# Optimization experiments

Hardware: AMD Instinct MI355X
Metric: run time of the kernel (lower is better)

Reference implementation:

```python
import jax, jax.numpy as jnp
import numpy as np

N = 50000          # nodes
E = 800000         # edges (before self-loops)
IN_CH = 16
HID = 32
HEADS = 4
NEG_SLOPE = 0.2    # PyG GATConv default leaky_relu slope


def add_self_loops(edge_index, n):
    loops = jnp.arange(n, dtype=edge_index.dtype)
    return jnp.concatenate([edge_index, jnp.stack([loops, loops])], axis=1)


def gat_layer(x, edge_index, W, a_src, a_dst, bias, heads, out_ch, concat):
    """PyG-style GATConv: gather -> attention logits -> segment softmax over dst -> scatter."""
    n = x.shape[0]
    h = (x @ W).reshape(n, heads, out_ch)            # [N, H, C]
    src, dst = edge_index[0], edge_index[1]          # messages flow src -> dst
    alpha_src = (h * a_src).sum(-1)                  # [N, H]
    alpha_dst = (h * a_dst).sum(-1)                  # [N, H]
    e = jax.nn.leaky_relu(alpha_src[src] + alpha_dst[dst], NEG_SLOPE)  # [Etot, H]
    # numerically stable segment softmax over incoming edges of each dst node
    e_max = jax.ops.segment_max(e, dst, num_segments=n)
    e_exp = jnp.exp(e - e_max[dst])
    denom = jax.ops.segment_sum(e_exp, dst, num_segments=n)
    alpha = e_exp / (denom[dst] + 1e-16)             # [Etot, H]
    out = jax.ops.segment_sum(h[src] * alpha[..., None], dst, num_segments=n)  # [N, H, C]
    out = out.reshape(n, heads * out_ch) if concat else out.mean(axis=1)
    return out + bias


def setup_inputs() -> dict:
    key = jax.random.key(0)
    ks = jax.random.split(key, 10)
    x = jax.random.normal(ks[0], (N, IN_CH), dtype=jnp.float32)
    edge_index = jax.random.randint(ks[1], (2, E), 0, N, dtype=jnp.int64)
    s = 0.1
    W1 = jax.random.normal(ks[2], (IN_CH, HEADS * HID), dtype=jnp.float32) * s
    a_src1 = jax.random.normal(ks[3], (1, HEADS, HID), dtype=jnp.float32) * s
    a_dst1 = jax.random.normal(ks[4], (1, HEADS, HID), dtype=jnp.float32) * s
    b1 = jnp.zeros((HEADS * HID,), dtype=jnp.float32)
    W2 = jax.random.normal(ks[5], (HEADS * HID, 2), dtype=jnp.float32) * s
    a_src2 = jax.random.normal(ks[6], (1, 1, 2), dtype=jnp.float32) * s
    a_dst2 = jax.random.normal(ks[7], (1, 1, 2), dtype=jnp.float32) * s
    b2 = jnp.zeros((2,), dtype=jnp.float32)
    return {"x": x, "edge_index": edge_index,
            "W1": W1, "a_src1": a_src1, "a_dst1": a_dst1, "b1": b1,
            "W2": W2, "a_src2": a_src2, "a_dst2": a_dst2, "b2": b2}


def reference(x, edge_index, W1, a_src1, a_dst1, b1, W2, a_src2, a_dst2, b2):
    ei = add_self_loops(edge_index, x.shape[0])
    h = gat_layer(x, ei, W1, a_src1, a_dst1, b1, HEADS, HID, concat=True)
    h = jax.nn.relu(h)
    out = gat_layer(h, ei, W2, a_src2, a_dst2, b2, 1, 2, concat=False)
    return out
```

## Files before the change

kernel.cpp:

```cpp
#include <hip/hip_runtime.h>
#include <hip/hip_bf16.h>

#define N_NODES 50000
#define N_EDGES 800000
#define ETOT    (N_EDGES + N_NODES)
#define STRIDE  64
#define IN_CH   16
#define HID     32
#define HEADS   4
#define C1      (HEADS * HID)
#define NEG     0.2f
#define NSLICE  8
#define SLICE_N (N_NODES / NSLICE)
#define CAPB    112640

#define DEG_BLOCKS  ((ETOT / 4 + 255) / 256)
#define FILL2_PARTS 110
#define FILL2_BLOCKS (NSLICE * FILL2_PARTS)
#define FILLL_BLOCKS (NSLICE * DEG_BLOCKS)
#define NGROUPS     (N_NODES / 4)
#define H1_BLOCKS   2048

typedef unsigned short u16;
typedef unsigned int   u32;

__device__ __forceinline__ float bf2f(u16 b) {
    return __uint_as_float(((u32)b) << 16);
}

__device__ __forceinline__ u16 f2bf(float f) {
    __hip_bfloat16 hb = __float2bfloat16(f);
    return *(u16*)&hb;
}

__device__ __forceinline__ int clampn(int v) {
    return v < 0 ? 0 : (v >= N_NODES ? N_NODES - 1 : v);
}

__device__ __forceinline__ int eidx(const int* ei, int e, int i64, int which) {
    int v = i64 ? ei[2 * (which * N_EDGES + e)] : ei[which * N_EDGES + e];
    return clampn(v);
}

__device__ __forceinline__ float cvt(const void* src, int i, int bf) {
    return bf ? bf2f(((const u16*)src)[i]) : ((const float*)src)[i];
}

__device__ __forceinline__ int probe_bf_wave(const u16* xb) {
    int l = threadIdx.x & 63;
    int my = 0;
#pragma unroll
    for (int k = 0; k < 4; k++) {
        float f = bf2f(xb[l * 4 + k]);
        float a = fabsf(f);
        if (f == 0.0f || (a > 9.5e-7f && a < 1.05e6f)) my++;
    }
#pragma unroll
    for (int m = 32; m; m >>= 1) my += __shfl_xor(my, m);
    return my >= 224;
}

__device__ __forceinline__ int probe_i64_wave(const int* ei32) {
    int l = threadIdx.x & 63;
    int nz = (l < 32 && ei32[2 * l + 1] != 0) ? 1 : 0;
#pragma unroll
    for (int m = 32; m; m >>= 1) nz += __shfl_xor(nz, m);
    return nz == 0;
}

__device__ __forceinline__ void dev_bucket(const int* __restrict__ ei,
                                           u32* __restrict__ gcnt,
                                           u32* __restrict__ gbuf,
                                           u32* sbuf, u32* scnt, u32* sseg,
                                           u32* sbase, int blk) {
    int i64 = probe_i64_wave(ei);
    if (threadIdx.x < NSLICE) scnt[threadIdx.x] = 0;
    __syncthreads();
    int e0 = (blk * 256 + (int)threadIdx.x) * 4;
    int valid = (e0 < ETOT);
    int bkt[4], pos[4]; u32 pk[4];
    if (valid) {
#pragma unroll
        for (int j = 0; j < 4; j++) {
            int e = e0 + j, s, d;
            if (e < N_EDGES) { s = eidx(ei, e, i64, 0); d = eidx(ei, e, i64, 1); }
            else             { s = d = e - N_EDGES; }
            int b = d / SLICE_N;
            bkt[j] = b;
            pk[j]  = ((u32)s << 16) | (u32)(d - b * SLICE_N);
            pos[j] = (int)atomicAdd(&scnt[b], 1u);
        }
    }
    __syncthreads();
    if (threadIdx.x == 0) {
        u32 run = 0;
        for (int b = 0; b < NSLICE; b++) { sseg[b] = run; run += scnt[b]; }
    }
    __syncthreads();
    if (threadIdx.x < NSLICE)
        sbase[threadIdx.x] = atomicAdd(&gcnt[threadIdx.x * 16], scnt[threadIdx.x]);
    if (valid) {
#pragma unroll
        for (int j = 0; j < 4; j++) sbuf[sseg[bkt[j]] + pos[j]] = pk[j];
    }
    __syncthreads();
#pragma unroll
    for (int b = 0; b < NSLICE; b++) {
        u32 cb = scnt[b], sb = sseg[b], gb = sbase[b];
        for (u32 i = threadIdx.x; i < cb; i += 256) {
            u32 o = gb + i;
            if (o < CAPB) gbuf[(size_t)b * CAPB + o] = sbuf[sb + i];
        }
    }
}

__device__ __forceinline__ void dev_fill2(const u32* __restrict__ gcnt,
                                          const u32* __restrict__ gbuf,
                                          int* __restrict__ degs,
                                          u16* __restrict__ csr, int blk) {
    int s = blk & (NSLICE - 1);
    int part = blk >> 3;
    u32 cnt = gcnt[s * 16]; if (cnt > CAPB) cnt = CAPB;
    u32 i0 = ((u32)part * 256 + (u32)threadIdx.x) * 4;
    if (i0 >= cnt) return;
    const u32* buf = gbuf + (size_t)s * CAPB;
    u32 pk[4]; int nv;
    if (i0 + 4 <= cnt) {
        uint4 q = *(const uint4*)(buf + i0);
        pk[0] = q.x; pk[1] = q.y; pk[2] = q.z; pk[3] = q.w; nv = 4;
    } else {
        nv = (int)(cnt - i0);
#pragma unroll
        for (int j = 0; j < 4; j++) if (j < nv) pk[j] = buf[i0 + j];
    }
    int base = s * SLICE_N;
#pragma unroll
    for (int j = 0; j < 4; j++) {
        if (j < nv) {
            int dst = base + (int)(pk[j] & 0xFFFFu);
            u32 r = (u32)atomicAdd(&degs[dst], 1) + 1u;
            if (r < STRIDE) csr[(size_t)dst * STRIDE + r] = (u16)(pk[j] >> 16);
        }
    }
}

__launch_bounds__(256)
__global__ void k_fill2(const u32* __restrict__ gcnt, const u32* __restrict__ gbuf,
                        int* __restrict__ degs, u16* __restrict__ csr) {
    dev_fill2(gcnt, gbuf, degs, csr, blockIdx.x);
}

__device__ __forceinline__ void dev_degfill(const int* __restrict__ ei,
                                            int* __restrict__ degs,
                                            u16* __restrict__ csr, int blk) {
    int slice = blk & (NSLICE - 1);
    int chunk = blk >> 3;
    int i64 = probe_i64_wave(ei);
    int e0 = (chunk * 256 + (int)threadIdx.x) * 4;
    if (e0 >= ETOT) return;
    int lo = slice * SLICE_N, hi = lo + SLICE_N;
    int s[4], d[4];
#pragma unroll
    for (int j = 0; j < 4; j++) {
        int e = e0 + j;
        if (e < N_EDGES) { s[j] = eidx(ei, e, i64, 0); d[j] = eidx(ei, e, i64, 1); }
        else             { s[j] = d[j] = e - N_EDGES; }
    }
#pragma unroll
    for (int j = 0; j < 4; j++) {
        if (d[j] >= lo && d[j] < hi) {
            u32 r = (u32)atomicAdd(&degs[d[j]], 1) + 1u;
            if (r < STRIDE) csr[(size_t)d[j] * STRIDE + r] = (u16)s[j];
        }
    }
}

__device__ __forceinline__ void dev_h1(const void* __restrict__ x,
                                       const void* __restrict__ W1,
                                       const void* __restrict__ a_s,
                                       const void* __restrict__ a_d,
                                       u32* __restrict__ h1u,
                                       float* __restrict__ as1,
                                       float* __restrict__ ad1, int blk) {
    int bf = probe_bf_wave((const u16*)x);
    if (blk == 0 && threadIdx.x < 4) as1[N_NODES * 4 + threadIdx.x] = -1e30f;
    if (blk == 0 && threadIdx.x >= 64 && threadIdx.x < 128)
        h1u[N_NODES * 64 + (threadIdx.x - 64)] = 0;

    int w = threadIdx.x >> 6, l = threadIdx.x & 63;

    float wa[IN_CH], wb[IN_CH];
    if (bf) {
        const u32* w32 = (const u32*)W1;
#pragma unroll
        for (int k = 0; k < IN_CH; k++) {
            u32 v = w32[k * 64 + l];
            wa[k] = bf2f((u16)(v & 0xFFFF));
            wb[k] = bf2f((u16)(v >> 16));
        }
    } else {
        const float2* w64 = (const float2*)W1;
#pragma unroll
        for (int k = 0; k < IN_CH; k++) {
            float2 v = w64[k * 64 + l];
            wa[k] = v.x; wb[k] = v.y;
        }
    }
    float asa, asb, ada, adb;
    if (bf) {
        u32 vs = ((const u32*)a_s)[l], vd = ((const u32*)a_d)[l];
        asa = bf2f((u16)(vs & 0xFFFF)); asb = bf2f((u16)(vs >> 16));
        ada = bf2f((u16)(vd & 0xFFFF)); adb = bf2f((u16)(vd >> 16));
    } else {
        float2 vs = ((const float2*)a_s)[l], vd = ((const float2*)a_d)[l];
        asa = vs.x; asb = vs.y; ada = vd.x; adb = vd.y;
    }

    for (int g = blk; g < NGROUPS; g += H1_BLOCKS) {
        int n = g * 4 + w;
        float xr[IN_CH];
        if (bf) {
            const uint4* xp = (const uint4*)((const u16*)x + (size_t)n * IN_CH);
            uint4 q0 = xp[0], q1 = xp[1];
            u32 qq[8] = {q0.x, q0.y, q0.z, q0.w, q1.x, q1.y, q1.z, q1.w};
#pragma unroll
            for (int k = 0; k < 8; k++) {
                xr[2 * k]     = bf2f((u16)(qq[k] & 0xFFFF));
                xr[2 * k + 1] = bf2f((u16)(qq[k] >> 16));
            }
        } else {
            const float4* xp = (const float4*)((const float*)x + (size_t)n * IN_CH);
#pragma unroll
            for (int k = 0; k < 4; k++) {
                float4 q = xp[k];
                xr[4 * k] = q.x; xr[4 * k + 1] = q.y;
                xr[4 * k + 2] = q.z; xr[4 * k + 3] = q.w;
            }
        }
        float acc0 = 0.f, acc1 = 0.f;
#pragma unroll
        for (int k = 0; k < IN_CH; k++) {
            acc0 += xr[k] * wa[k];
            acc1 += xr[k] * wb[k];
        }
        h1u[n * 64 + l] = (u32)f2bf(acc0) | ((u32)f2bf(acc1) << 16);

        float ps = acc0 * asa + acc1 * asb;
        float pd = acc0 * ada + acc1 * adb;
#pragma unroll
        for (int m = 8; m; m >>= 1) { ps += __shfl_xor(ps, m); pd += __shfl_xor(pd, m); }
        if ((l & 15) == 0) {
            int hd = l >> 4;
            as1[n * 4 + hd] = ps;
            ad1[n * 4 + hd] = pd;
        }
    }
}

__launch_bounds__(256)
__global__ void k_bucket_h1(const void* __restrict__ x, const int* __restrict__ ei,
                            const void* __restrict__ W1, const void* __restrict__ a_s,
                            const void* __restrict__ a_d,
                            u32* __restrict__ gcnt, u32* __restrict__ gbuf,
                            u32* __restrict__ h1u, float* __restrict__ as1,
                            float* __restrict__ ad1) {
    __shared__ u32 sbuf[1024];
    __shared__ u32 scnt[NSLICE], sseg[NSLICE], sbase[NSLICE];
    if (blockIdx.x < DEG_BLOCKS) {
        dev_bucket(ei, gcnt, gbuf, sbuf, scnt, sseg, sbase, blockIdx.x);
        return;
    }
    dev_h1(x, W1, a_s, a_d, h1u, as1, ad1, blockIdx.x - DEG_BLOCKS);
}

__launch_bounds__(256)
__global__ void k_fill_h1_legacy(const void* __restrict__ x, const int* __restrict__ ei,
                                 const void* __restrict__ W1, const void* __restrict__ a_s,
                                 const void* __restrict__ a_d,
                                 int* __restrict__ degs, u16* __restrict__ csr,
                                 u32* __restrict__ h1u, float* __restrict__ as1,
                                 float* __restrict__ ad1) {
    if (blockIdx.x < FILLL_BLOCKS) { dev_degfill(ei, degs, csr, blockIdx.x); return; }
    dev_h1(x, W1, a_s, a_d, h1u, as1, ad1, blockIdx.x - FILLL_BLOCKS);
}

__launch_bounds__(256)
__global__ void k_gather1(const void* __restrict__ x,
                          const int* __restrict__ degs, const u16* __restrict__ csr,
                          const u32* __restrict__ h1u,
                          const float* __restrict__ as1, const float* __restrict__ ad1,
                          const void* __restrict__ b1, const void* __restrict__ W2,
                          const void* __restrict__ a2s, const void* __restrict__ a2d,
                          float* __restrict__ h2, float* __restrict__ as2,
                          float* __restrict__ ad2) {
    int bf = probe_bf_wave((const u16*)x);
    int n = blockIdx.x * 4 + (threadIdx.x >> 6);
    int l = threadIdx.x & 63;
    int hd = l >> 4;
    int je = l & 7;
    int jh = (l >> 3) & 3;
    float advb = ad1[n * 4 + jh];
    int deg = degs[n] + 1;
    deg = deg > STRIDE ? STRIDE : deg;
    int nb = (deg + 7) >> 3;
    const u16* row = csr + (size_t)n * STRIDE;
    float acc0 = 0.f, acc1 = 0.f, swd = 0.f;

    int se = (int)row[je];
    if (se >= N_NODES) se = N_NODES;
    for (int b = 0; b < nb; b++) {
        int se_next = 0xFFFF;
        if (b + 1 < nb) se_next = (int)row[(b + 1) * 8 + je];
        float t = as1[se * 4 + jh] + advb;
        t = t > 0.f ? t : NEG * t;
        float wm = __expf(t);
        swd += wm;
#pragma unroll
        for (int j = 0; j < 8; j++) {
            int   sj = __shfl(se, j);
            float wj = __shfl(wm, hd * 8 + j);
            u32 p = h1u[sj * 64 + l];
            acc0 += wj * bf2f((u16)(p & 0xFFFF));
            acc1 += wj * bf2f((u16)(p >> 16));
        }
        se = se_next >= N_NODES ? N_NODES : se_next;
    }

    swd += __shfl_xor(swd, 1);
    swd += __shfl_xor(swd, 2);
    swd += __shfl_xor(swd, 4);
    float sw = __shfl(swd, hd * 8);

    float inv = 1.0f / sw;
    float v0 = acc0 * inv + cvt(b1, 2 * l, bf);
    float v1 = acc1 * inv + cvt(b1, 2 * l + 1, bf);
    v0 = v0 > 0.f ? v0 : 0.f;
    v1 = v1 > 0.f ? v1 : 0.f;
    float p0 = v0 * cvt(W2, 4 * l,     bf) + v1 * cvt(W2, 4 * l + 2, bf);
    float p1 = v0 * cvt(W2, 4 * l + 1, bf) + v1 * cvt(W2, 4 * l + 3, bf);
#pragma unroll
    for (int d = 32; d; d >>= 1) { p0 += __shfl_down(p0, d); p1 += __shfl_down(p1, d); }
    if (l == 0) {
        h2[n * 2] = p0; h2[n * 2 + 1] = p1;
        as2[n] = p0 * cvt(a2s, 0, bf) + p1 * cvt(a2s, 1, bf);
        ad2[n] = p0 * cvt(a2d, 0, bf) + p1 * cvt(a2d, 1, bf);
    }
}

__launch_bounds__(256)
__global__ void k_gather2(const void* __restrict__ x,
                          const int* __restrict__ degs, const u16* __restrict__ csr,
                          const float* __restrict__ h2, const float* __restrict__ as2,
                          const float* __restrict__ ad2, const void* __restrict__ b2,
                          void* __restrict__ out) {
    int bf = probe_bf_wave((const u16*)x);
    int n = blockIdx.x * 16 + (threadIdx.x >> 4);
    int g = threadIdx.x & 15;
    float adv = ad2[n], a0 = 0.f, a1 = 0.f, sw = 0.f;
    int deg = degs[n] + 1;
    deg = deg > STRIDE ? STRIDE : deg;
    const u16* row = csr + (size_t)n * STRIDE;
    for (int k = g; k < deg; k += 16) {
        int s = (int)row[k];
        float lg = as2[s] + adv;
        lg = lg > 0.f ? lg : NEG * lg;
        float w = __expf(lg);
        float2 hv = ((const float2*)h2)[s];
        a0 += w * hv.x;
        a1 += w * hv.y;
        sw += w;
    }
#pragma unroll
    for (int m = 8; m; m >>= 1) {
        a0 += __shfl_xor(a0, m); a1 += __shfl_xor(a1, m); sw += __shfl_xor(sw, m);
    }
    if (g == 0) {
        float inv = 1.0f / sw;
        float o0 = a0 * inv + cvt(b2, 0, bf);
        float o1 = a1 * inv + cvt(b2, 1, bf);
        if (bf) {
            ((u32*)out)[n] = (u32)f2bf(o0) | ((u32)f2bf(o1) << 16);
        } else {
            ((float2*)out)[n] = make_float2(o0, o1);
        }
    }
}

extern "C" void kernel_launch(void* const* d_in, const int* in_sizes, int n_in,
                              void* d_out, int out_size, void* d_ws, size_t ws_size,
                              hipStream_t stream) {
    const void* x    = d_in[0];
    const int*  ei   = (const int*)d_in[1];
    const void* W1   = d_in[2];
    const void* a_s1 = d_in[3];
    const void* a_d1 = d_in[4];
    const void* b1   = d_in[5];
    const void* W2   = d_in[6];
    const void* a_s2 = d_in[7];
    const void* a_d2 = d_in[8];
    const void* b2   = d_in[9];

    char* p = (char*)d_ws;
    int*   degs = (int*)p;     p += ((size_t)N_NODES * 4 + 255) & ~255;
    u16*   csr  = (u16*)p;     p += (size_t)N_NODES * STRIDE * 2;
    size_t init_bytes = (size_t)(p - (char*)d_ws);
    u32*   gcnt = (u32*)p;     p += 512;
    u32*   h1u  = (u32*)p;     p += (size_t)(N_NODES + 1) * 64 * 4;
    float* as1  = (float*)p;   p += (size_t)(N_NODES + 1) * HEADS * 4;
    float* ad1  = (float*)p;   p += (size_t)N_NODES * HEADS * 4;
    float* h2   = (float*)p;   p += (size_t)N_NODES * 2 * 4;
    float* as2  = (float*)p;   p += (size_t)N_NODES * 4;
    float* ad2  = (float*)p;   p += (size_t)N_NODES * 4;
    u32*   gbuf = (u32*)p;     p += (size_t)NSLICE * CAPB * 4;
    size_t need = (size_t)(p - (char*)d_ws);

    hipMemsetAsync(degs, 0xFF, init_bytes, stream);

    if (ws_size >= need) {
        hipMemsetAsync(gcnt, 0x00, 512, stream);
        k_bucket_h1<<<DEG_BLOCKS + H1_BLOCKS, 256, 0, stream>>>(
            x, ei, W1, a_s1, a_d1, gcnt, gbuf, h1u, as1, ad1);
        k_fill2<<<FILL2_BLOCKS, 256, 0, stream>>>(gcnt, gbuf, degs, csr);
    } else {
        k_fill_h1_legacy<<<FILLL_BLOCKS + H1_BLOCKS, 256, 0, stream>>>(
            x, ei, W1, a_s1, a_d1, degs, csr, h1u, as1, ad1);
    }
    k_gather1<<<N_NODES / 4, 256, 0, stream>>>(
        x, degs, csr, h1u, as1, ad1, b1, W2, a_s2, a_d2, h2, as2, ad2);
    k_gather2<<<N_NODES / 16, 256, 0, stream>>>(
        x, degs, csr, h2, as2, ad2, b2, d_out);
}
```

Before: 212.0 us.

## Aggregate raw input features before projection instead of gathering projected h1

Layer-1 aggregation now gathers 16-channel input rows x[src] and applies W1 after the weighted sum, using linearity (sum alpha*xW = (sum alpha*x)W per head). The 128-wide bf16 h1 buffer is no longer written or read, which cuts gather bandwidth per edge. Each lane group handles one head with 16 edges per batch, and the W1 matmul runs once per node inside the gather kernel. The legacy small-workspace fallback path is removed, so the bucket path is now unconditional. The x gather uses 2- or 4-byte scalar loads per lane, and the weight registers add pressure.

After: 258.6 us. 1.22x slower.

```diff
diff --git a/kernel.cpp b/kernel.cpp
--- a/kernel.cpp
+++ b/kernel.cpp
@@ -17,7 +17,6 @@
 #define DEG_BLOCKS  ((ETOT / 4 + 255) / 256)
 #define FILL2_PARTS 110
 #define FILL2_BLOCKS (NSLICE * FILL2_PARTS)
-#define FILLL_BLOCKS (NSLICE * DEG_BLOCKS)
 #define NGROUPS     (N_NODES / 4)
 #define H1_BLOCKS   2048
 
@@ -150,43 +149,13 @@
     dev_fill2(gcnt, gbuf, degs, csr, blockIdx.x);
 }
 
-__device__ __forceinline__ void dev_degfill(const int* __restrict__ ei,
-                                            int* __restrict__ degs,
-                                            u16* __restrict__ csr, int blk) {
-    int slice = blk & (NSLICE - 1);
-    int chunk = blk >> 3;
-    int i64 = probe_i64_wave(ei);
-    int e0 = (chunk * 256 + (int)threadIdx.x) * 4;
-    if (e0 >= ETOT) return;
-    int lo = slice * SLICE_N, hi = lo + SLICE_N;
-    int s[4], d[4];
-#pragma unroll
-    for (int j = 0; j < 4; j++) {
-        int e = e0 + j;
-        if (e < N_EDGES) { s[j] = eidx(ei, e, i64, 0); d[j] = eidx(ei, e, i64, 1); }
-        else             { s[j] = d[j] = e - N_EDGES; }
-    }
-#pragma unroll
-    for (int j = 0; j < 4; j++) {
-        if (d[j] >= lo && d[j] < hi) {
-            u32 r = (u32)atomicAdd(&degs[d[j]], 1) + 1u;
-            if (r < STRIDE) csr[(size_t)d[j] * STRIDE + r] = (u16)s[j];
-        }
-    }
-}
-
 __device__ __forceinline__ void dev_h1(const void* __restrict__ x,
                                        const void* __restrict__ W1,
                                        const void* __restrict__ a_s,
                                        const void* __restrict__ a_d,
-                                       u32* __restrict__ h1u,
                                        float* __restrict__ as1,
                                        float* __restrict__ ad1, int blk) {
     int bf = probe_bf_wave((const u16*)x);
-    if (blk == 0 && threadIdx.x < 4) as1[N_NODES * 4 + threadIdx.x] = -1e30f;
-    if (blk == 0 && threadIdx.x >= 64 && threadIdx.x < 128)
-        h1u[N_NODES * 64 + (threadIdx.x - 64)] = 0;
-
     int w = threadIdx.x >> 6, l = threadIdx.x & 63;
 
     float wa[IN_CH], wb[IN_CH];
@@ -243,8 +212,6 @@
             acc0 += xr[k] * wa[k];
             acc1 += xr[k] * wb[k];
         }
-        h1u[n * 64 + l] = (u32)f2bf(acc0) | ((u32)f2bf(acc1) << 16);
-
         float ps = acc0 * asa + acc1 * asb;
         float pd = acc0 * ada + acc1 * adb;
 #pragma unroll
@@ -262,33 +229,21 @@
                             const void* __restrict__ W1, const void* __restrict__ a_s,
                             const void* __restrict__ a_d,
                             u32* __restrict__ gcnt, u32* __restrict__ gbuf,
-                            u32* __restrict__ h1u, float* __restrict__ as1,
-                            float* __restrict__ ad1) {
+                            float* __restrict__ as1, float* __restrict__ ad1) {
     __shared__ u32 sbuf[1024];
     __shared__ u32 scnt[NSLICE], sseg[NSLICE], sbase[NSLICE];
     if (blockIdx.x < DEG_BLOCKS) {
         dev_bucket(ei, gcnt, gbuf, sbuf, scnt, sseg, sbase, blockIdx.x);
         return;
     }
-    dev_h1(x, W1, a_s, a_d, h1u, as1, ad1, blockIdx.x - DEG_BLOCKS);
-}
-
-__launch_bounds__(256)
-__global__ void k_fill_h1_legacy(const void* __restrict__ x, const int* __restrict__ ei,
-                                 const void* __restrict__ W1, const void* __restrict__ a_s,
-                                 const void* __restrict__ a_d,
-                                 int* __restrict__ degs, u16* __restrict__ csr,
-                                 u32* __restrict__ h1u, float* __restrict__ as1,
-                                 float* __restrict__ ad1) {
-    if (blockIdx.x < FILLL_BLOCKS) { dev_degfill(ei, degs, csr, blockIdx.x); return; }
-    dev_h1(x, W1, a_s, a_d, h1u, as1, ad1, blockIdx.x - FILLL_BLOCKS);
+    dev_h1(x, W1, a_s, a_d, as1, ad1, blockIdx.x - DEG_BLOCKS);
 }
 
 __launch_bounds__(256)
 __global__ void k_gather1(const void* __restrict__ x,
                           const int* __restrict__ degs, const u16* __restrict__ csr,
-                          const u32* __restrict__ h1u,
                           const float* __restrict__ as1, const float* __restrict__ ad1,
+                          const void* __restrict__ W1,
                           const void* __restrict__ b1, const void* __restrict__ W2,
                           const void* __restrict__ a2s, const void* __restrict__ a2d,
                           float* __restrict__ h2, float* __restrict__ as2,
@@ -296,44 +251,71 @@
     int bf = probe_bf_wave((const u16*)x);
     int n = blockIdx.x * 4 + (threadIdx.x >> 6);
     int l = threadIdx.x & 63;
-    int hd = l >> 4;
-    int je = l & 7;
-    int jh = (l >> 3) & 3;
-    float advb = ad1[n * 4 + jh];
+    int h = l >> 4;
+    int k = l & 15;
+    int g16 = l & 48;
+
+    float wa[IN_CH], wb[IN_CH];
+    if (bf) {
+        const u32* w32 = (const u32*)W1;
+#pragma unroll
+        for (int kk = 0; kk < IN_CH; kk++) {
+            u32 v = w32[kk * 64 + l];
+            wa[kk] = bf2f((u16)(v & 0xFFFF));
+            wb[kk] = bf2f((u16)(v >> 16));
+        }
+    } else {
+        const float2* w64 = (const float2*)W1;
+#pragma unroll
+        for (int kk = 0; kk < IN_CH; kk++) {
+            float2 v = w64[kk * 64 + l];
+            wa[kk] = v.x; wb[kk] = v.y;
+        }
+    }
+
+    float adv = ad1[n * 4 + h];
     int deg = degs[n] + 1;
     deg = deg > STRIDE ? STRIDE : deg;
-    int nb = (deg + 7) >> 3;
+    int nb = (deg + 15) >> 4;
     const u16* row = csr + (size_t)n * STRIDE;
-    float acc0 = 0.f, acc1 = 0.f, swd = 0.f;
-
-    int se = (int)row[je];
-    if (se >= N_NODES) se = N_NODES;
+
+    float acc = 0.f, swd = 0.f;
     for (int b = 0; b < nb; b++) {
-        int se_next = 0xFFFF;
-        if (b + 1 < nb) se_next = (int)row[(b + 1) * 8 + je];
-        float t = as1[se * 4 + jh] + advb;
-        t = t > 0.f ? t : NEG * t;
-        float wm = __expf(t);
+        int se = (int)row[b * 16 + k];
+        int sx; float wm;
+        if (se >= N_NODES) { sx = 0; wm = 0.f; }
+        else {
+            sx = se;
+            float t = as1[se * 4 + h] + adv;
+            t = t > 0.f ? t : NEG * t;
+            wm = __expf(t);
+        }
         swd += wm;
 #pragma unroll
-        for (int j = 0; j < 8; j++) {
-            int   sj = __shfl(se, j);
-            float wj = __shfl(wm, hd * 8 + j);
-            u32 p = h1u[sj * 64 + l];
-            acc0 += wj * bf2f((u16)(p & 0xFFFF));
-            acc1 += wj * bf2f((u16)(p >> 16));
-        }
-        se = se_next >= N_NODES ? N_NODES : se_next;
+        for (int j = 0; j < 16; j++) {
+            int   sj = __shfl(sx, g16 + j);
+            float wj = __shfl(wm, g16 + j);
+            float xv = bf ? bf2f(((const u16*)x)[(size_t)sj * IN_CH + k])
+                          : ((const float*)x)[(size_t)sj * IN_CH + k];
+            acc += wj * xv;
+        }
     }
 
     swd += __shfl_xor(swd, 1);
     swd += __shfl_xor(swd, 2);
     swd += __shfl_xor(swd, 4);
-    float sw = __shfl(swd, hd * 8);
-
-    float inv = 1.0f / sw;
-    float v0 = acc0 * inv + cvt(b1, 2 * l, bf);
-    float v1 = acc1 * inv + cvt(b1, 2 * l + 1, bf);
+    swd += __shfl_xor(swd, 8);
+    float aggn = acc * (1.0f / swd);
+
+    float o0 = 0.f, o1 = 0.f;
+#pragma unroll
+    for (int kk = 0; kk < IN_CH; kk++) {
+        float a = __shfl(aggn, g16 + kk);
+        o0 += a * wa[kk];
+        o1 += a * wb[kk];
+    }
+    float v0 = o0 + cvt(b1, 2 * l, bf);
+    float v1 = o1 + cvt(b1, 2 * l + 1, bf);
     v0 = v0 > 0.f ? v0 : 0.f;
     v1 = v1 > 0.f ? v1 : 0.f;
     float p0 = v0 * cvt(W2, 4 * l,     bf) + v1 * cvt(W2, 4 * l + 2, bf);
@@ -405,28 +387,21 @@
     u16*   csr  = (u16*)p;     p += (size_t)N_NODES * STRIDE * 2;
     size_t init_bytes = (size_t)(p - (char*)d_ws);
     u32*   gcnt = (u32*)p;     p += 512;
-    u32*   h1u  = (u32*)p;     p += (size_t)(N_NODES + 1) * 64 * 4;
-    float* as1  = (float*)p;   p += (size_t)(N_NODES + 1) * HEADS * 4;
+    float* as1  = (float*)p;   p += (size_t)N_NODES * HEADS * 4;
     float* ad1  = (float*)p;   p += (size_t)N_NODES * HEADS * 4;
     float* h2   = (float*)p;   p += (size_t)N_NODES * 2 * 4;
     float* as2  = (float*)p;   p += (size_t)N_NODES * 4;
     float* ad2  = (float*)p;   p += (size_t)N_NODES * 4;
     u32*   gbuf = (u32*)p;     p += (size_t)NSLICE * CAPB * 4;
-    size_t need = (size_t)(p - (char*)d_ws);
 
     hipMemsetAsync(degs, 0xFF, init_bytes, stream);
-
-    if (ws_size >= need) {
-        hipMemsetAsync(gcnt, 0x00, 512, stream);
-        k_bucket_h1<<<DEG_BLOCKS + H1_BLOCKS, 256, 0, stream>>>(
-            x, ei, W1, a_s1, a_d1, gcnt, gbuf, h1u, as1, ad1);
-        k_fill2<<<FILL2_BLOCKS, 256, 0, stream>>>(gcnt, gbuf, degs, csr);
-    } else {
-        k_fill_h1_legacy<<<FILLL_BLOCKS + H1_BLOCKS, 256, 0, stream>>>(
-            x, ei, W1, a_s1, a_d1, degs, csr, h1u, as1, ad1);
-    }
+    hipMemsetAsync(gcnt, 0x00, 512, stream);
+
+    k_bucket_h1<<<DEG_BLOCKS + H1_BLOCKS, 256, 0, stream>>>(
+        x, ei, W1, a_s1, a_d1, gcnt, gbuf, as1, ad1);
+    k_fill2<<<FILL2_BLOCKS, 256, 0, stream>>>(gcnt, gbuf, degs, csr);
     k_gather1<<<N_NODES / 4, 256, 0, stream>>>(
-        x, degs, csr, h1u, as1, ad1, b1, W2, a_s2, a_d2, h2, as2, ad2);
+        x, degs, csr, as1, ad1, W1, b1, W2, a_s2, a_d2, h2, as2, ad2);
     k_gather2<<<N_NODES / 16, 256, 0, stream>>>(
         x, degs, csr, h2, as2, ad2, b2, d_out);
 }
```
